# Kernel optimization log

Measured on AMD Instinct MI355X. Metric: run time of the kernel, lower is better.

Reference implementation:

```python
import jax, jax.numpy as jnp
import numpy as np

B = 16        # number of lists
N = 1024      # items per list (all equal)
D = 256       # feature dim (= dim_emb, need_embedding=False)


def setup_inputs() -> dict:
    key = jax.random.key(0)
    k1, k2, k3 = jax.random.split(key, 3)
    feats = jax.random.normal(k1, (B * N, D), dtype=jnp.float32)
    length = jnp.full((B,), N, dtype=jnp.int32)
    # Bilinear params: torch nn.Bilinear(d, d, 1) -> weight [1, d, d], bias [1]
    # xavier_uniform on the 3-d weight: bound = sqrt(6 / (fan_in + fan_out)) with
    # fan_in = d (last dim), fan_out = 1*d (per torch _calculate_fan_in_and_fan_out)
    bound = float(np.sqrt(6.0 / (D + D)))
    W_upper = jax.random.uniform(k2, (1, D, D), jnp.float32, -bound, bound)
    W_lower = jax.random.uniform(k3, (1, D, D), jnp.float32, -bound, bound)
    b_upper = jnp.zeros((1,), jnp.float32)
    b_lower = jnp.zeros((1,), jnp.float32)
    return {"feats": feats, "W_upper": W_upper, "b_upper": b_upper,
            "W_lower": W_lower, "b_lower": b_lower, "length": length}


def reference(feats, W_upper, b_upper, W_lower, b_lower, length):
    # nb_layers=0, need_embedding=False -> embedding and transformer are Identity.
    b = length.shape[0]
    n = feats.shape[0] // b  # equal-length lists -> static reshape
    d = feats.shape[-1]
    X = feats.reshape(b, n, d)  # [B, n, d]
    # For list i: repeated_feats_1 row (p*n + q) = x_p, repeated_feats_2 row = x_q,
    # so adjacency[p, q] = x_p^T W x_q + bias  (Bilinear with out=1).
    upper = jnp.einsum('bnd,de,bme->bnm', X, W_upper[0], X) + b_upper[0]
    lower = jnp.einsum('bnd,de,bme->bnm', X, W_lower[0], X) + b_lower[0]
    adj = jnp.triu(upper) + jnp.tril(lower, -1)  # [B, n, n]
    return adj
```

## Files before the change

kernel.cpp:

```cpp
#include <hip/hip_runtime.h>

#define BL 16
#define NL 1024
#define DD 256

typedef short bf16x8 __attribute__((ext_vector_type(8)));
typedef float f32x4 __attribute__((ext_vector_type(4)));

static __device__ __forceinline__ short f32_to_bf16(float f) {
  union { float f; unsigned u; } v; v.f = f;
  unsigned r = (v.u + 0x7FFFu + ((v.u >> 16) & 1u)) >> 16;
  return (short)r;
}

static __device__ __forceinline__ void g2l16(const short* g, short* l) {
  __builtin_amdgcn_global_load_lds(
      (const __attribute__((address_space(1))) void*)g,
      (__attribute__((address_space(3))) void*)l, 16, 0, 0);
}

__global__ __launch_bounds__(256) void k_prep(const float* __restrict__ X,
                                              const float* __restrict__ Wu,
                                              const float* __restrict__ Wl,
                                              short* __restrict__ Xb,
                                              short* __restrict__ WTu,
                                              short* __restrict__ WTl) {
  const int bid = blockIdx.x;
  if (bid < 4096) {
    int i = bid * 256 + threadIdx.x;
    const float4 v = ((const float4*)X)[i];
    short4 o;
    o.x = f32_to_bf16(v.x); o.y = f32_to_bf16(v.y);
    o.z = f32_to_bf16(v.z); o.w = f32_to_bf16(v.w);
    ((short4*)Xb)[i] = o;
  } else {
    const int id = bid - 4096;
    const int z = id >> 8, d = id & 255;
    const float* W = z ? Wl : Wu;
    short* WT = z ? WTl : WTu;
    const int e = threadIdx.x;
    WT[e * DD + d] = f32_to_bf16(W[d * DD + e]);
  }
}

__global__ __launch_bounds__(1024, 4) void k_fused(const short* __restrict__ Xb,
                                                   const short* __restrict__ WTu,
                                                   const short* __restrict__ WTl,
                                                   const float* __restrict__ bu_p,
                                                   const float* __restrict__ bl_p,
                                                   float* __restrict__ out) {
  __shared__ short Asw[64 * 256];
  __shared__ short Yu[64 * 256];
  __shared__ short Yl[64 * 256];

  const int bid = blockIdx.x;
  const int b = bid & 15, pt = bid >> 4;
  const int t = threadIdx.x, lane = t & 63, w = t >> 6;
  const int r = lane & 15, quad = lane >> 4;
  const size_t listoff = (size_t)b * NL * DD;
  const short* Ap = Xb + listoff + (size_t)pt * 64 * DD;

#pragma unroll
  for (int i = 0; i < 2; ++i) {
    const int c = i * 1024 + t;
    const int src = c ^ ((c >> 5) & 7);
    g2l16(Ap + src * 8, Asw + c * 8);
  }
  __syncthreads();

  {
    const int n0 = w * 16;
    f32x4 aU[4] = {}, aL[4] = {};
#pragma unroll
    for (int ks = 0; ks < 8; ++ks) {
      bf16x8 af[4];
#pragma unroll
      for (int mt = 0; mt < 4; ++mt) {
        const int row = mt * 16 + r;
        const int abyte = (row * 512 + ks * 64 + quad * 16) ^ ((row & 7) << 4);
        af[mt] = *(const bf16x8*)((const char*)Asw + abyte);
      }
      const int off = (n0 + r) * DD + ks * 32 + quad * 8;
      const bf16x8 bfu = *(const bf16x8*)(WTu + off);
      const bf16x8 bfl = *(const bf16x8*)(WTl + off);
#pragma unroll
      for (int mt = 0; mt < 4; ++mt) {
        aU[mt] = __builtin_amdgcn_mfma_f32_16x16x32_bf16(af[mt], bfu, aU[mt], 0, 0, 0);
        aL[mt] = __builtin_amdgcn_mfma_f32_16x16x32_bf16(af[mt], bfl, aL[mt], 0, 0, 0);
      }
    }
#pragma unroll
    for (int mt = 0; mt < 4; ++mt)
#pragma unroll
      for (int i = 0; i < 4; ++i) {
        const int row = mt * 16 + quad * 4 + i;
        const int col = n0 + r;
        const int byte = (row * 512 + col * 2) ^ ((row & 7) << 4);
        *(short*)((char*)Yu + byte) = f32_to_bf16(aU[mt][i]);
        *(short*)((char*)Yl + byte) = f32_to_bf16(aL[mt][i]);
      }
  }

  const float ub = bu_p[0], lb = bl_p[0];
  float* Ob = out + (size_t)b * NL * NL;
  const int p0 = pt * 64;
  const int qt = w, q0 = qt * 64;
  const short* Bg = Xb + listoff + (size_t)qt * 64 * DD;
  const float bias = (qt >= pt) ? ub : lb;

  auto loadB = [&](bf16x8 (&dst)[4], int ks) {
#pragma unroll
    for (int nt = 0; nt < 4; ++nt)
      dst[nt] = *(const bf16x8*)(Bg + (size_t)(nt * 16 + r) * DD + ks * 32 + quad * 8);
  };
  auto mmaStep = [&](const short* Y, const bf16x8 (&bf)[4], f32x4 (&ac)[4][4], int ks) {
#pragma unroll
    for (int mt = 0; mt < 4; ++mt) {
      const int row = mt * 16 + r;
      const int abyte = (row * 512 + ks * 64 + quad * 16) ^ ((row & 7) << 4);
      const bf16x8 af = *(const bf16x8*)((const char*)Y + abyte);
#pragma unroll
      for (int nt = 0; nt < 4; ++nt)
        ac[nt][mt] = __builtin_amdgcn_mfma_f32_16x16x32_bf16(bf[nt], af, ac[nt][mt], 0, 0, 0);
    }
  };

  bf16x8 bfA[4], bfB[4];
  loadB(bfA, 0);
  loadB(bfB, 1);
  __syncthreads();

  const short* YA = (qt >= pt) ? Yu : Yl;
  f32x4 acc[4][4] = {};
  mmaStep(YA, bfA, acc, 0);  loadB(bfA, 2);
  mmaStep(YA, bfB, acc, 1);  loadB(bfB, 3);
  mmaStep(YA, bfA, acc, 2);  loadB(bfA, 4);
  mmaStep(YA, bfB, acc, 3);  loadB(bfB, 5);
  mmaStep(YA, bfA, acc, 4);  loadB(bfA, 6);
  mmaStep(YA, bfB, acc, 5);  loadB(bfB, 7);
  mmaStep(YA, bfA, acc, 6);
  mmaStep(YA, bfB, acc, 7);

#pragma unroll
  for (int mt = 0; mt < 4; ++mt) {
    float* row = Ob + (size_t)(p0 + mt * 16 + r) * NL;
#pragma unroll
    for (int nt = 0; nt < 4; ++nt) {
      f32x4 v;
#pragma unroll
      for (int i = 0; i < 4; ++i) v[i] = acc[nt][mt][i] + bias;
      *(f32x4*)(row + q0 + nt * 16 + quad * 4) = v;
    }
  }

  if (qt == pt) {
    f32x4 accL[4][4] = {};
    loadB(bfA, 0);
    loadB(bfB, 1);
    mmaStep(Yl, bfA, accL, 0);  loadB(bfA, 2);
    mmaStep(Yl, bfB, accL, 1);  loadB(bfB, 3);
    mmaStep(Yl, bfA, accL, 2);  loadB(bfA, 4);
    mmaStep(Yl, bfB, accL, 3);  loadB(bfB, 5);
    mmaStep(Yl, bfA, accL, 4);  loadB(bfA, 6);
    mmaStep(Yl, bfB, accL, 5);  loadB(bfB, 7);
    mmaStep(Yl, bfA, accL, 6);
    mmaStep(Yl, bfB, accL, 7);
#pragma unroll
    for (int mt = 0; mt < 4; ++mt) {
      const int p = p0 + mt * 16 + r;
      float* row = Ob + (size_t)p * NL;
#pragma unroll
      for (int nt = 0; nt < 4; ++nt)
#pragma unroll
        for (int i = 0; i < 4; ++i) {
          const int q = q0 + nt * 16 + quad * 4 + i;
          if (q < p) row[q] = accL[nt][mt][i] + lb;
        }
    }
  }
}

extern "C" void kernel_launch(void* const* d_in, const int* in_sizes, int n_in,
                              void* d_out, int out_size, void* d_ws, size_t ws_size,
                              hipStream_t stream) {
  const float* feats = (const float*)d_in[0];
  const float* Wu    = (const float*)d_in[1];
  const float* bu    = (const float*)d_in[2];
  const float* Wl    = (const float*)d_in[3];
  const float* bl    = (const float*)d_in[4];
  float* out = (float*)d_out;

  char* ws = (char*)d_ws;
  short* Xb  = (short*)(ws);
  short* WTu = (short*)(ws + (size_t)8 * 1024 * 1024);
  short* WTl = (short*)(ws + (size_t)8 * 1024 * 1024 + DD * DD * 2);

  k_prep<<<4096 + 512, 256, 0, stream>>>(feats, Wu, Wl, Xb, WTu, WTl);

  k_fused<<<256, 1024, 0, stream>>>(Xb, WTu, WTl, bu, bl, out);
}
```

Before: 130.1 us.

## Split each p-tile across two 512-thread blocks and alias Yl onto A buffer

The fused kernel now launches 512 blocks of 512 threads, each handling half of the q-tiles for a 64-row p-tile. Each block recomputes the full X·W projection with eight waves, each producing 32 columns. The lower projection is written into the A-staging buffer after a barrier, which cuts LDS per block from three buffers to two so more blocks can reside per CU. Scheduling barriers are added between the MMA steps and the B loads to pin the intended interleave. The cost is that the projection GEMM is now computed twice per p-tile.

```diff
diff --git a/kernel.cpp b/kernel.cpp
--- a/kernel.cpp
+++ b/kernel.cpp
@@ -43,68 +43,76 @@
   }
 }
 
-__global__ __launch_bounds__(1024, 4) void k_fused(const short* __restrict__ Xb,
-                                                   const short* __restrict__ WTu,
-                                                   const short* __restrict__ WTl,
-                                                   const float* __restrict__ bu_p,
-                                                   const float* __restrict__ bl_p,
-                                                   float* __restrict__ out) {
+__global__ __launch_bounds__(512, 4) void k_fused(const short* __restrict__ Xb,
+                                                  const short* __restrict__ WTu,
+                                                  const short* __restrict__ WTl,
+                                                  const float* __restrict__ bu_p,
+                                                  const float* __restrict__ bl_p,
+                                                  float* __restrict__ out) {
   __shared__ short Asw[64 * 256];
   __shared__ short Yu[64 * 256];
-  __shared__ short Yl[64 * 256];
 
   const int bid = blockIdx.x;
-  const int b = bid & 15, pt = bid >> 4;
+  const int b = bid & 15, z = bid >> 4;
+  const int pt = z >> 1, qh = z & 1;
   const int t = threadIdx.x, lane = t & 63, w = t >> 6;
   const int r = lane & 15, quad = lane >> 4;
   const size_t listoff = (size_t)b * NL * DD;
   const short* Ap = Xb + listoff + (size_t)pt * 64 * DD;
 
 #pragma unroll
-  for (int i = 0; i < 2; ++i) {
-    const int c = i * 1024 + t;
+  for (int i = 0; i < 4; ++i) {
+    const int c = i * 512 + t;
     const int src = c ^ ((c >> 5) & 7);
     g2l16(Ap + src * 8, Asw + c * 8);
   }
   __syncthreads();
 
-  {
-    const int n0 = w * 16;
-    f32x4 aU[4] = {}, aL[4] = {};
-#pragma unroll
-    for (int ks = 0; ks < 8; ++ks) {
-      bf16x8 af[4];
-#pragma unroll
-      for (int mt = 0; mt < 4; ++mt) {
-        const int row = mt * 16 + r;
-        const int abyte = (row * 512 + ks * 64 + quad * 16) ^ ((row & 7) << 4);
-        af[mt] = *(const bf16x8*)((const char*)Asw + abyte);
+  const int n0 = w * 32;
+  f32x4 aU[4][2] = {}, aL[4][2] = {};
+#pragma unroll
+  for (int ks = 0; ks < 8; ++ks) {
+    bf16x8 af[4];
+#pragma unroll
+    for (int mt = 0; mt < 4; ++mt) {
+      const int row = mt * 16 + r;
+      const int abyte = (row * 512 + ks * 64 + quad * 16) ^ ((row & 7) << 4);
+      af[mt] = *(const bf16x8*)((const char*)Asw + abyte);
+    }
+    bf16x8 bfu[2], bfl[2];
+#pragma unroll
+    for (int nf = 0; nf < 2; ++nf) {
+      const int off = (n0 + nf * 16 + r) * DD + ks * 32 + quad * 8;
+      bfu[nf] = *(const bf16x8*)(WTu + off);
+      bfl[nf] = *(const bf16x8*)(WTl + off);
+    }
+#pragma unroll
+    for (int mt = 0; mt < 4; ++mt)
+#pragma unroll
+      for (int nf = 0; nf < 2; ++nf) {
+        aU[mt][nf] = __builtin_amdgcn_mfma_f32_16x16x32_bf16(af[mt], bfu[nf], aU[mt][nf], 0, 0, 0);
+        aL[mt][nf] = __builtin_amdgcn_mfma_f32_16x16x32_bf16(af[mt], bfl[nf], aL[mt][nf], 0, 0, 0);
       }
-      const int off = (n0 + r) * DD + ks * 32 + quad * 8;
-      const bf16x8 bfu = *(const bf16x8*)(WTu + off);
-      const bf16x8 bfl = *(const bf16x8*)(WTl + off);
-#pragma unroll
-      for (int mt = 0; mt < 4; ++mt) {
-        aU[mt] = __builtin_amdgcn_mfma_f32_16x16x32_bf16(af[mt], bfu, aU[mt], 0, 0, 0);
-        aL[mt] = __builtin_amdgcn_mfma_f32_16x16x32_bf16(af[mt], bfl, aL[mt], 0, 0, 0);
-      }
-    }
-#pragma unroll
-    for (int mt = 0; mt < 4; ++mt)
+  }
+  __syncthreads();
+
+#pragma unroll
+  for (int mt = 0; mt < 4; ++mt)
+#pragma unroll
+    for (int nf = 0; nf < 2; ++nf)
 #pragma unroll
       for (int i = 0; i < 4; ++i) {
         const int row = mt * 16 + quad * 4 + i;
-        const int col = n0 + r;
+        const int col = n0 + nf * 16 + r;
         const int byte = (row * 512 + col * 2) ^ ((row & 7) << 4);
-        *(short*)((char*)Yu + byte) = f32_to_bf16(aU[mt][i]);
-        *(short*)((char*)Yl + byte) = f32_to_bf16(aL[mt][i]);
+        *(short*)((char*)Yu + byte) = f32_to_bf16(aU[mt][nf][i]);
+        *(short*)((char*)Asw + byte) = f32_to_bf16(aL[mt][nf][i]);
       }
-  }
 
   const float ub = bu_p[0], lb = bl_p[0];
   float* Ob = out + (size_t)b * NL * NL;
   const int p0 = pt * 64;
-  const int qt = w, q0 = qt * 64;
+  const int qt = qh * 8 + w, q0 = qt * 64;
   const short* Bg = Xb + listoff + (size_t)qt * 64 * DD;
   const float bias = (qt >= pt) ? ub : lb;
 
@@ -118,26 +126,27 @@
     for (int mt = 0; mt < 4; ++mt) {
       const int row = mt * 16 + r;
       const int abyte = (row * 512 + ks * 64 + quad * 16) ^ ((row & 7) << 4);
-      const bf16x8 af = *(const bf16x8*)((const char*)Y + abyte);
+      const bf16x8 af2 = *(const bf16x8*)((const char*)Y + abyte);
 #pragma unroll
       for (int nt = 0; nt < 4; ++nt)
-        ac[nt][mt] = __builtin_amdgcn_mfma_f32_16x16x32_bf16(bf[nt], af, ac[nt][mt], 0, 0, 0);
+        ac[nt][mt] = __builtin_amdgcn_mfma_f32_16x16x32_bf16(bf[nt], af2, ac[nt][mt], 0, 0, 0);
     }
   };
 
   bf16x8 bfA[4], bfB[4];
   loadB(bfA, 0);
   loadB(bfB, 1);
+  __builtin_amdgcn_sched_barrier(0);
   __syncthreads();
 
-  const short* YA = (qt >= pt) ? Yu : Yl;
+  const short* YA = (qt >= pt) ? Yu : Asw;
   f32x4 acc[4][4] = {};
-  mmaStep(YA, bfA, acc, 0);  loadB(bfA, 2);
-  mmaStep(YA, bfB, acc, 1);  loadB(bfB, 3);
-  mmaStep(YA, bfA, acc, 2);  loadB(bfA, 4);
-  mmaStep(YA, bfB, acc, 3);  loadB(bfB, 5);
-  mmaStep(YA, bfA, acc, 4);  loadB(bfA, 6);
-  mmaStep(YA, bfB, acc, 5);  loadB(bfB, 7);
+  mmaStep(YA, bfA, acc, 0);  loadB(bfA, 2);  __builtin_amdgcn_sched_barrier(0);
+  mmaStep(YA, bfB, acc, 1);  loadB(bfB, 3);  __builtin_amdgcn_sched_barrier(0);
+  mmaStep(YA, bfA, acc, 2);  loadB(bfA, 4);  __builtin_amdgcn_sched_barrier(0);
+  mmaStep(YA, bfB, acc, 3);  loadB(bfB, 5);  __builtin_amdgcn_sched_barrier(0);
+  mmaStep(YA, bfA, acc, 4);  loadB(bfA, 6);  __builtin_amdgcn_sched_barrier(0);
+  mmaStep(YA, bfB, acc, 5);  loadB(bfB, 7);  __builtin_amdgcn_sched_barrier(0);
   mmaStep(YA, bfA, acc, 6);
   mmaStep(YA, bfB, acc, 7);
 
@@ -157,14 +166,14 @@
     f32x4 accL[4][4] = {};
     loadB(bfA, 0);
     loadB(bfB, 1);
-    mmaStep(Yl, bfA, accL, 0);  loadB(bfA, 2);
-    mmaStep(Yl, bfB, accL, 1);  loadB(bfB, 3);
-    mmaStep(Yl, bfA, accL, 2);  loadB(bfA, 4);
-    mmaStep(Yl, bfB, accL, 3);  loadB(bfB, 5);
-    mmaStep(Yl, bfA, accL, 4);  loadB(bfA, 6);
-    mmaStep(Yl, bfB, accL, 5);  loadB(bfB, 7);
-    mmaStep(Yl, bfA, accL, 6);
-    mmaStep(Yl, bfB, accL, 7);
+    mmaStep(Asw, bfA, accL, 0);  loadB(bfA, 2);
+    mmaStep(Asw, bfB, accL, 1);  loadB(bfB, 3);
+    mmaStep(Asw, bfA, accL, 2);  loadB(bfA, 4);
+    mmaStep(Asw, bfB, accL, 3);  loadB(bfB, 5);
+    mmaStep(Asw, bfA, accL, 4);  loadB(bfA, 6);
+    mmaStep(Asw, bfB, accL, 5);  loadB(bfB, 7);
+    mmaStep(Asw, bfA, accL, 6);
+    mmaStep(Asw, bfB, accL, 7);
 #pragma unroll
     for (int mt = 0; mt < 4; ++mt) {
       const int p = p0 + mt * 16 + r;
@@ -197,5 +206,5 @@
 
   k_prep<<<4096 + 512, 256, 0, stream>>>(feats, Wu, Wl, Xb, WTu, WTl);
 
-  k_fused<<<256, 1024, 0, stream>>>(Xb, WTu, WTl, bu, bl, out);
-}
+  k_fused<<<512, 512, 0, stream>>>(Xb, WTu, WTl, bu, bl, out);
+}
```

After: 145.6 us. 1.12x slower.
